# Kernel tuning notes

Hardware: AMD Instinct MI355X
Metric: run time of the kernel (lower is better)

The kernel has to match this reference:

```python
import jax, jax.numpy as jnp
import numpy as np

B, D, E, H, T = 16384, 32, 8, 64, 10  # batch, state_dim, n_experts, hidden, time points
TEMP = 1.0  # gating temperature


def setup_inputs() -> dict:
    key = jax.random.key(0)
    ks = jax.random.split(key, 12)
    w = lambda k, shape, fan_in: (jax.random.normal(k, shape, jnp.float32) / np.sqrt(fan_in)).astype(jnp.float32)
    return {
        "x0": jax.random.normal(ks[0], (B, D), jnp.float32),
        "t_span": jnp.linspace(0.0, 1.0, T).astype(jnp.float32),
        # per-expert time-conditioned MLP: (x, t) -> H -> H -> D
        "W1": w(ks[1], (E, D + 1, H), D + 1), "b1": jnp.zeros((E, H), jnp.float32),
        "W2": w(ks[2], (E, H, H), H),          "b2": jnp.zeros((E, H), jnp.float32),
        "W3": w(ks[3], (E, H, D), H),          "b3": jnp.zeros((E, D), jnp.float32),
        # gating MLP on concat(x, dx_init): 2D -> H -> E
        "Gw1": w(ks[4], (2 * D, H), 2 * D), "Gb1": jnp.zeros((H,), jnp.float32),
        "Gw2": w(ks[5], (H, E), H),         "Gb2": jnp.zeros((E,), jnp.float32),
    }


def _dyn(t, x, W1, b1, W2, b2, W3, b3, Gw1, Gb1, Gw2, Gb2):
    # AME-ODE training-path dynamics: uniform-weighted init, gate, weighted sum
    inp = jnp.concatenate([x, jnp.ones((x.shape[0], 1), x.dtype) * t], axis=-1)  # [B, D+1]
    h = jnp.tanh(jnp.einsum('bi,eih->beh', inp, W1) + b1)
    h = jnp.tanh(jnp.einsum('beh,ehg->beg', h, W2) + b2)
    f = jnp.einsum('beg,egd->bed', h, W3) + b3          # all-expert dynamics [B, E, D]
    dx_init = f.mean(axis=1)                             # uniform weights 1/E
    g = jnp.tanh(jnp.concatenate([x, dx_init], -1) @ Gw1 + Gb1)
    wgt = jax.nn.softmax((g @ Gw2 + Gb2) / TEMP, axis=-1)  # [B, E]
    return jnp.einsum('be,bed->bd', wgt, f)


def reference(x0, t_span, W1, b1, W2, b2, W3, b3, Gw1, Gb1, Gw2, Gb2):
    params = (W1, b1, W2, b2, W3, b3, Gw1, Gb1, Gw2, Gb2)

    def step(x, ts):
        t0, t1 = ts[0], ts[1]
        dt = t1 - t0
        k1 = _dyn(t0, x, *params)
        k2 = _dyn(t0 + 0.5 * dt, x + 0.5 * dt * k1, *params)
        k3 = _dyn(t0 + 0.5 * dt, x + 0.5 * dt * k2, *params)
        k4 = _dyn(t1, x + dt * k3, *params)
        xn = x + (dt / 6.0) * (k1 + 2.0 * k2 + 2.0 * k3 + k4)
        return xn, xn

    pairs = jnp.stack([t_span[:-1], t_span[1:]], axis=1)  # [T-1, 2]
    _, traj = jax.lax.scan(step, x0, pairs)               # [T-1, B, D]
    traj = jnp.concatenate([x0[None], traj], axis=0)       # [T, B, D]
    return jnp.transpose(traj, (1, 0, 2))                  # [B, T, D]
```

## Files before the change

kernel.cpp:

```cpp
#include <hip/hip_runtime.h>
#include <hip/hip_bf16.h>

typedef unsigned int u32;
typedef unsigned short u16;
typedef __attribute__((ext_vector_type(8))) short short8;
typedef __attribute__((ext_vector_type(4))) float f32x4;
typedef __attribute__((ext_vector_type(4))) u32 u32x4;
typedef __attribute__((ext_vector_type(2))) u32 u32x2;

#define DD 32
#define EE 8
#define HH 64
#define TT 10
#define BATCH 16384
#define EPB 64
#define DYN_LDS 75776

#if __has_builtin(__builtin_amdgcn_exp2f)
#define EXP2F(x) __builtin_amdgcn_exp2f(x)
#else
#define EXP2F(x) __builtin_exp2f(x)
#endif

__device__ __forceinline__ float fast_tanh(float x) {
  float e = EXP2F(x * 2.885390082f);
  return 1.f - 2.f * __builtin_amdgcn_rcpf(e + 1.f);
}
__device__ __forceinline__ u16 f2b_rn(float v) {
  return (u16)((__float_as_uint(v) + 0x8000u) >> 16);
}
__device__ __forceinline__ u32 pack2_rn(float a, float b) {
  return __builtin_amdgcn_perm(__float_as_uint(b) + 0x8000u,
                               __float_as_uint(a) + 0x8000u, 0x07060302u);
}
__device__ __forceinline__ float unp_lo(u32 p) { return __uint_as_float(p << 16); }
__device__ __forceinline__ float unp_hi(u32 p) { return __uint_as_float(p & 0xffff0000u); }
__device__ __forceinline__ short8 lds_frag(const u32* p) {
  u32x4 v = *(const u32x4*)p;
  return __builtin_bit_cast(short8, v);
}
__device__ __forceinline__ f32x4 bcast4(float v) { f32x4 c; c[0]=v; c[1]=v; c[2]=v; c[3]=v; return c; }

__global__ __launch_bounds__(512) void ame_ode_kernel(
    const float* __restrict__ x0, const float* __restrict__ tspan,
    const float* __restrict__ W1, const float* __restrict__ b1,
    const float* __restrict__ W2, const float* __restrict__ b2,
    const float* __restrict__ W3, const float* __restrict__ b3,
    const float* __restrict__ Gw1, const float* __restrict__ Gb1,
    const float* __restrict__ Gw2, const float* __restrict__ Gb2,
    float* __restrict__ out)
{
  extern __shared__ __align__(16) u32 dynbuf[];
  u32*  const xdb = dynbuf;
  u32*  const fsb = dynbuf + 1280;
  u32*  const hs  = dynbuf + 9728;

  const int tid  = threadIdx.x;
  const int lane = tid & 63;
  const int l15  = lane & 15;
  const int quad = lane >> 4;
  const int e    = __builtin_amdgcn_readfirstlane(tid >> 6);

  const int el = lane >> 3;
  const int q8 = lane & 7;
  const int gr = e * 8 + el;
  const int gb = blockIdx.x * EPB + gr;

  const float* W1f = W1 + e * (DD + 1) * HH;
  const float* b1f = b1 + e * HH;
  const float* W2f = W2 + e * HH * HH;
  const float* b2f = b2 + e * HH;
  const float* W3f = W3 + e * HH * DD;
  const float* b3f = b3 + e * DD;

  short8 bw1[4], bw2[2][4], bw3[2][2];
  #pragma unroll
  for (int nt = 0; nt < 4; nt++)
    #pragma unroll
    for (int j = 0; j < 8; j++)
      bw1[nt][j] = (short)f2b_rn(W1f[(quad * 8 + j) * HH + nt * 16 + l15]);
  #pragma unroll
  for (int ks = 0; ks < 2; ks++)
    #pragma unroll
    for (int nt = 0; nt < 4; nt++)
      #pragma unroll
      for (int j = 0; j < 8; j++)
        bw2[ks][nt][j] = (short)f2b_rn(W2f[(ks * 32 + quad * 8 + j) * HH + nt * 16 + l15]);
  #pragma unroll
  for (int ks = 0; ks < 2; ks++)
    #pragma unroll
    for (int dt2 = 0; dt2 < 2; dt2++)
      #pragma unroll
      for (int j = 0; j < 8; j++)
        bw3[ks][dt2][j] = (short)f2b_rn(W3f[(ks * 32 + quad * 8 + j) * DD + dt2 * 16 + l15]);

  short8 bg1x[4], bg1f[4];
  float gb1v[4];
  #pragma unroll
  for (int nt = 0; nt < 4; nt++) {
    #pragma unroll
    for (int j = 0; j < 8; j++) {
      bg1x[nt][j] = (short)f2b_rn(Gw1[(quad * 8 + j) * HH + nt * 16 + l15]);
      bg1f[nt][j] = (short)f2b_rn(0.125f * Gw1[(DD + quad * 8 + j) * HH + nt * 16 + l15]);
    }
    gb1v[nt] = Gb1[nt * 16 + l15];
  }

  short8 bg2[2];
  #pragma unroll
  for (int ks = 0; ks < 2; ks++)
    #pragma unroll
    for (int j = 0; j < 8; j++)
      bg2[ks][j] = (short)((l15 < 8) ? f2b_rn(Gw2[(ks * 32 + quad * 8 + j) * EE + l15]) : 0);
  const float gb2v = (l15 < 8) ? Gb2[l15] : 0.f;

  u32 c1p[4], c2p[2], c3p;
  #pragma unroll
  for (int nt = 0; nt < 4; nt++)
    c1p[nt] = pack2_rn(b1f[nt * 16 + l15], W1f[DD * HH + nt * 16 + l15]);
  #pragma unroll
  for (int p = 0; p < 2; p++)
    c2p[p] = pack2_rn(b2f[(2 * p) * 16 + l15], b2f[(2 * p + 1) * 16 + l15]);
  c3p = pack2_rn(b3f[l15], b3f[16 + l15]);

  float xst[4], xacc[4];
  {
    const float4 v = *(const float4*)(x0 + gb * DD + q8 * 4);
    xst[0] = v.x; xst[1] = v.y; xst[2] = v.z; xst[3] = v.w;
    xacc[0] = v.x; xacc[1] = v.y; xacc[2] = v.z; xacc[3] = v.w;
    u32x2 p; p.x = pack2_rn(v.x, v.y); p.y = pack2_rn(v.z, v.w);
    *(u32x2*)&xdb[gr * 20 + q8 * 2] = p;
    *(float4*)(out + gb * TT * DD + q8 * 4) = v;
  }
  __syncthreads();

  u16*  const fw16 = (u16*)fsb;
  u32*  const hsw  = hs + e * 1152;
  u16*  const uw16 = (u16*)hsw;
  float* const wscr = (float*)(hsw + 576);

  #pragma unroll 1
  for (int step = 0; step < TT - 1; step++) {
    const float t0 = tspan[step];
    const float t1 = tspan[step + 1];
    const float dt = t1 - t0;

    #pragma unroll 1
    for (int s = 0; s < 4; s++) {
      const float tcur = (s == 0) ? t0 : ((s == 3) ? t1 : t0 + 0.5f * dt);

      f32x4 c1i[4];
      #pragma unroll
      for (int nt = 0; nt < 4; nt++)
        c1i[nt] = bcast4(__builtin_fmaf(tcur, unp_hi(c1p[nt]), unp_lo(c1p[nt])));

      #pragma unroll 2
      for (int mt = 0; mt < 4; mt++) {
        u32* const hw   = hsw + (mt & 1) * 576;
        u16* const hw16 = (u16*)hw;

        const short8 a1 = lds_frag(&xdb[(mt * 16 + l15) * 20 + quad * 4]);
        f32x4 h1a[4];
        #pragma unroll
        for (int nt = 0; nt < 4; nt++)
          h1a[nt] = __builtin_amdgcn_mfma_f32_16x16x32_bf16(a1, bw1[nt], c1i[nt], 0, 0, 0);
        #pragma unroll
        for (int nt = 0; nt < 4; nt++)
          #pragma unroll
          for (int r = 0; r < 4; r++)
            hw16[(quad * 4 + r) * 72 + nt * 16 + l15] = f2b_rn(fast_tanh(h1a[nt][r]));

        f32x4 h2a[4];
        #pragma unroll
        for (int nt = 0; nt < 4; nt++)
          h2a[nt] = bcast4((nt & 1) ? unp_hi(c2p[nt >> 1]) : unp_lo(c2p[nt >> 1]));
        #pragma unroll
        for (int ks = 0; ks < 2; ks++) {
          const short8 a2 = lds_frag(&hw[l15 * 36 + ks * 16 + quad * 4]);
          #pragma unroll
          for (int nt = 0; nt < 4; nt++)
            h2a[nt] = __builtin_amdgcn_mfma_f32_16x16x32_bf16(a2, bw2[ks][nt], h2a[nt], 0, 0, 0);
        }
        #pragma unroll
        for (int nt = 0; nt < 4; nt++)
          #pragma unroll
          for (int r = 0; r < 4; r++)
            hw16[(quad * 4 + r) * 72 + nt * 16 + l15] = f2b_rn(fast_tanh(h2a[nt][r]));

        f32x4 fa[2];
        #pragma unroll
        for (int dt2 = 0; dt2 < 2; dt2++)
          fa[dt2] = bcast4(dt2 ? unp_hi(c3p) : unp_lo(c3p));
        #pragma unroll
        for (int ks = 0; ks < 2; ks++) {
          const short8 a3 = lds_frag(&hw[l15 * 36 + ks * 16 + quad * 4]);
          #pragma unroll
          for (int dt2 = 0; dt2 < 2; dt2++)
            fa[dt2] = __builtin_amdgcn_mfma_f32_16x16x32_bf16(a3, bw3[ks][dt2], fa[dt2], 0, 0, 0);
        }
        #pragma unroll
        for (int dt2 = 0; dt2 < 2; dt2++)
          #pragma unroll
          for (int r = 0; r < 4; r++)
            fw16[(mt * 16 + quad * 4 + r) * 264 + e * 32 + dt2 * 16 + l15] = f2b_rn(fa[dt2][r]);
      }

      f32x4 u4[4];
      {
        const short8 ax = lds_frag(&xdb[(e * 8 + (l15 & 7)) * 20 + quad * 4]);
        #pragma unroll
        for (int nt = 0; nt < 4; nt++)
          u4[nt] = __builtin_amdgcn_mfma_f32_16x16x32_bf16(ax, bg1x[nt], bcast4(gb1v[nt]), 0, 0, 0);
      }
      __syncthreads();

      #pragma unroll
      for (int kb = 0; kb < 8; kb++) {
        const short8 af = lds_frag(&fsb[(e * 8 + (l15 & 7)) * 132 + kb * 16 + quad * 4]);
        #pragma unroll
        for (int nt = 0; nt < 4; nt++)
          u4[nt] = __builtin_amdgcn_mfma_f32_16x16x32_bf16(af, bg1f[nt], u4[nt], 0, 0, 0);
      }
      #pragma unroll
      for (int nt = 0; nt < 4; nt++)
        #pragma unroll
        for (int r = 0; r < 4; r++)
          uw16[(quad * 4 + r) * 72 + nt * 16 + l15] = f2b_rn(fast_tanh(u4[nt][r]));

      f32x4 lv = bcast4(gb2v);
      #pragma unroll
      for (int ks = 0; ks < 2; ks++) {
        const short8 ag = lds_frag(&hsw[l15 * 36 + ks * 16 + quad * 4]);
        lv = __builtin_amdgcn_mfma_f32_16x16x32_bf16(ag, bg2[ks], lv, 0, 0, 0);
      }

      float wgt[4];
      #pragma unroll
      for (int r = 0; r < 4; r++) {
        const float p = __expf(lv[r]);
        float ssum = p + __shfl_xor(p, 1);
        ssum += __shfl_xor(ssum, 2);
        ssum += __shfl_xor(ssum, 4);
        wgt[r] = p * __builtin_amdgcn_rcpf(ssum);
      }
      if (quad < 2 && l15 < 8) {
        #pragma unroll
        for (int r = 0; r < 4; r++)
          wscr[(quad * 4 + r) * 8 + l15] = wgt[r];
      }
      const f32x4 w0 = *(const f32x4*)&wscr[el * 8];
      const f32x4 w1 = *(const f32x4*)&wscr[el * 8 + 4];

      float kc[4] = {0.f, 0.f, 0.f, 0.f};
      #pragma unroll
      for (int j = 0; j < EE; j++) {
        const float wg = (j < 4) ? w0[j] : w1[j - 4];
        const u32x2 pf = *(const u32x2*)&fsb[gr * 132 + j * 16 + q8 * 2];
        kc[0] = __builtin_fmaf(wg, unp_lo(pf.x), kc[0]);
        kc[1] = __builtin_fmaf(wg, unp_hi(pf.x), kc[1]);
        kc[2] = __builtin_fmaf(wg, unp_lo(pf.y), kc[2]);
        kc[3] = __builtin_fmaf(wg, unp_hi(pf.y), kc[3]);
      }

      const float wk = (s == 1 || s == 2) ? 2.f : 1.f;
      const float ak = dt * (1.f / 6.f) * wk;
      #pragma unroll
      for (int q = 0; q < 4; q++) xacc[q] = __builtin_fmaf(ak, kc[q], xacc[q]);

      float xn[4];
      if (s < 3) {
        const float cn = (s == 2) ? dt : 0.5f * dt;
        #pragma unroll
        for (int q = 0; q < 4; q++) xn[q] = __builtin_fmaf(cn, kc[q], xst[q]);
      } else {
        #pragma unroll
        for (int q = 0; q < 4; q++) { xst[q] = xacc[q]; xn[q] = xacc[q]; }
        float4 o; o.x = xn[0]; o.y = xn[1]; o.z = xn[2]; o.w = xn[3];
        *(float4*)(out + (gb * TT + step + 1) * DD + q8 * 4) = o;
      }
      u32x2 p; p.x = pack2_rn(xn[0], xn[1]); p.y = pack2_rn(xn[2], xn[3]);
      *(u32x2*)&xdb[gr * 20 + q8 * 2] = p;

      __syncthreads();
    }
  }
}

extern "C" void kernel_launch(void* const* d_in, const int* in_sizes, int n_in,
                              void* d_out, int out_size, void* d_ws, size_t ws_size,
                              hipStream_t stream)
{
  const float* x0    = (const float*)d_in[0];
  const float* tspan = (const float*)d_in[1];
  const float* W1  = (const float*)d_in[2];
  const float* b1  = (const float*)d_in[3];
  const float* W2  = (const float*)d_in[4];
  const float* b2  = (const float*)d_in[5];
  const float* W3  = (const float*)d_in[6];
  const float* b3  = (const float*)d_in[7];
  const float* Gw1 = (const float*)d_in[8];
  const float* Gb1 = (const float*)d_in[9];
  const float* Gw2 = (const float*)d_in[10];
  const float* Gb2 = (const float*)d_in[11];

  (void)hipFuncSetAttribute((const void*)ame_ode_kernel,
                            hipFuncAttributeMaxDynamicSharedMemorySize, DYN_LDS);

  ame_ode_kernel<<<BATCH / EPB, 512, DYN_LDS, stream>>>(
      x0, tspan, W1, b1, W2, b2, W3, b3, Gw1, Gb1, Gw2, Gb2, (float*)d_out);
}
```

Measured before the change: 343.5 us.

## Repartition gating GEMM across warps to remove redundant row computation

Before, each warp computed the gating first layer for 16 A-rows of which only 8 were real (rows l15&7 duplicated), across all 4 N-tiles. Now each of the 8 warps computes one 16-row M-tile by two N-tiles of the gating hidden layer. The results go to a new shared LDS buffer, and after an extra barrier each warp reads its rows back for the second gating layer. This halves the redundant MFMA work and the gating weight registers, at the cost of an added __syncthreads and more LDS.

```diff
diff --git a/kernel.cpp b/kernel.cpp
--- a/kernel.cpp
+++ b/kernel.cpp
@@ -14,7 +14,7 @@
 #define TT 10
 #define BATCH 16384
 #define EPB 64
-#define DYN_LDS 75776
+#define DYN_LDS 84992
 
 #if __has_builtin(__builtin_amdgcn_exp2f)
 #define EXP2F(x) __builtin_amdgcn_exp2f(x)
@@ -53,7 +53,8 @@
   extern __shared__ __align__(16) u32 dynbuf[];
   u32*  const xdb = dynbuf;
   u32*  const fsb = dynbuf + 1280;
-  u32*  const hs  = dynbuf + 9728;
+  u32*  const usb = dynbuf + 9728;
+  u32*  const hs  = dynbuf + 12032;
 
   const int tid  = threadIdx.x;
   const int lane = tid & 63;
@@ -94,17 +95,18 @@
       for (int j = 0; j < 8; j++)
         bw3[ks][dt2][j] = (short)f2b_rn(W3f[(ks * 32 + quad * 8 + j) * DD + dt2 * 16 + l15]);
 
-  short8 bg1x[4], bg1f[4];
-  float gb1v[4];
-  #pragma unroll
-  for (int nt = 0; nt < 4; nt++) {
+  const int g1mt = e & 3;
+  const int g1n0 = (e >> 2) * 2;
+  short8 bg1x[2], bg1f[2];
+  #pragma unroll
+  for (int ni = 0; ni < 2; ni++)
     #pragma unroll
     for (int j = 0; j < 8; j++) {
-      bg1x[nt][j] = (short)f2b_rn(Gw1[(quad * 8 + j) * HH + nt * 16 + l15]);
-      bg1f[nt][j] = (short)f2b_rn(0.125f * Gw1[(DD + quad * 8 + j) * HH + nt * 16 + l15]);
+      bg1x[ni][j] = (short)f2b_rn(Gw1[(quad * 8 + j) * HH + (g1n0 + ni) * 16 + l15]);
+      bg1f[ni][j] = (short)f2b_rn(0.125f * Gw1[(DD + quad * 8 + j) * HH + (g1n0 + ni) * 16 + l15]);
     }
-    gb1v[nt] = Gb1[nt * 16 + l15];
-  }
+  const float gb1a = Gb1[g1n0 * 16 + l15];
+  const float gb1b = Gb1[(g1n0 + 1) * 16 + l15];
 
   short8 bg2[2];
   #pragma unroll
@@ -125,19 +127,18 @@
 
   float xst[4], xacc[4];
   {
-    const float4 v = *(const float4*)(x0 + gb * DD + q8 * 4);
+    const float4 v = *(const float4*)(x0 + gb * DD + 4 * q8);
     xst[0] = v.x; xst[1] = v.y; xst[2] = v.z; xst[3] = v.w;
     xacc[0] = v.x; xacc[1] = v.y; xacc[2] = v.z; xacc[3] = v.w;
     u32x2 p; p.x = pack2_rn(v.x, v.y); p.y = pack2_rn(v.z, v.w);
     *(u32x2*)&xdb[gr * 20 + q8 * 2] = p;
-    *(float4*)(out + gb * TT * DD + q8 * 4) = v;
+    *(float4*)(out + gb * TT * DD + 4 * q8) = v;
   }
   __syncthreads();
 
-  u16*  const fw16 = (u16*)fsb;
-  u32*  const hsw  = hs + e * 1152;
-  u16*  const uw16 = (u16*)hsw;
-  float* const wscr = (float*)(hsw + 576);
+  u16* const fw16 = (u16*)fsb;
+  u16* const us16 = (u16*)usb;
+  u32* const hsw  = hs + e * 1152;
 
   #pragma unroll 1
   for (int step = 0; step < TT - 1; step++) {
@@ -204,83 +205,83 @@
           for (int r = 0; r < 4; r++)
             fw16[(mt * 16 + quad * 4 + r) * 264 + e * 32 + dt2 * 16 + l15] = f2b_rn(fa[dt2][r]);
       }
-
-      f32x4 u4[4];
+      __syncthreads();
+
       {
-        const short8 ax = lds_frag(&xdb[(e * 8 + (l15 & 7)) * 20 + quad * 4]);
-        #pragma unroll
-        for (int nt = 0; nt < 4; nt++)
-          u4[nt] = __builtin_amdgcn_mfma_f32_16x16x32_bf16(ax, bg1x[nt], bcast4(gb1v[nt]), 0, 0, 0);
+        f32x4 u0 = bcast4(gb1a), u1 = bcast4(gb1b);
+        const int mg = g1mt * 16 + l15;
+        const short8 ax = lds_frag(&xdb[mg * 20 + quad * 4]);
+        u0 = __builtin_amdgcn_mfma_f32_16x16x32_bf16(ax, bg1x[0], u0, 0, 0, 0);
+        u1 = __builtin_amdgcn_mfma_f32_16x16x32_bf16(ax, bg1x[1], u1, 0, 0, 0);
+        #pragma unroll
+        for (int kb = 0; kb < 8; kb++) {
+          const short8 af = lds_frag(&fsb[mg * 132 + kb * 16 + quad * 4]);
+          u0 = __builtin_amdgcn_mfma_f32_16x16x32_bf16(af, bg1f[0], u0, 0, 0, 0);
+          u1 = __builtin_amdgcn_mfma_f32_16x16x32_bf16(af, bg1f[1], u1, 0, 0, 0);
+        }
+        #pragma unroll
+        for (int r = 0; r < 4; r++) {
+          us16[(g1mt * 16 + quad * 4 + r) * 72 + g1n0 * 16 + l15]       = f2b_rn(fast_tanh(u0[r]));
+          us16[(g1mt * 16 + quad * 4 + r) * 72 + (g1n0 + 1) * 16 + l15] = f2b_rn(fast_tanh(u1[r]));
+        }
       }
       __syncthreads();
 
-      #pragma unroll
-      for (int kb = 0; kb < 8; kb++) {
-        const short8 af = lds_frag(&fsb[(e * 8 + (l15 & 7)) * 132 + kb * 16 + quad * 4]);
-        #pragma unroll
-        for (int nt = 0; nt < 4; nt++)
-          u4[nt] = __builtin_amdgcn_mfma_f32_16x16x32_bf16(af, bg1f[nt], u4[nt], 0, 0, 0);
+      {
+        f32x4 lv = bcast4(gb2v);
+        #pragma unroll
+        for (int ks = 0; ks < 2; ks++) {
+          const short8 ag = lds_frag(&usb[(e * 8 + (l15 & 7)) * 36 + ks * 16 + quad * 4]);
+          lv = __builtin_amdgcn_mfma_f32_16x16x32_bf16(ag, bg2[ks], lv, 0, 0, 0);
+        }
+        float wgt[4];
+        #pragma unroll
+        for (int r = 0; r < 4; r++) {
+          const float p = __expf(lv[r]);
+          float ssum = p + __shfl_xor(p, 1);
+          ssum += __shfl_xor(ssum, 2);
+          ssum += __shfl_xor(ssum, 4);
+          wgt[r] = p * __builtin_amdgcn_rcpf(ssum);
+        }
+        float* const wscr = (float*)(hsw + 576);
+        if (quad < 2 && l15 < 8) {
+          #pragma unroll
+          for (int r = 0; r < 4; r++)
+            wscr[((quad * 4 + r) & 7) * 8 + l15] = wgt[r];
+        }
+        const f32x4 w0 = *(const f32x4*)&wscr[el * 8];
+        const f32x4 w1 = *(const f32x4*)&wscr[el * 8 + 4];
+
+        float kc[4] = {0.f, 0.f, 0.f, 0.f};
+        #pragma unroll
+        for (int j = 0; j < EE; j++) {
+          const float wg = (j < 4) ? w0[j] : w1[j - 4];
+          const u32x2 pf = *(const u32x2*)&fsb[gr * 132 + j * 16 + q8 * 2];
+          kc[0] = __builtin_fmaf(wg, unp_lo(pf.x), kc[0]);
+          kc[1] = __builtin_fmaf(wg, unp_hi(pf.x), kc[1]);
+          kc[2] = __builtin_fmaf(wg, unp_lo(pf.y), kc[2]);
+          kc[3] = __builtin_fmaf(wg, unp_hi(pf.y), kc[3]);
+        }
+
+        const float wk = (s == 1 || s == 2) ? 2.f : 1.f;
+        const float ak = dt * (1.f / 6.f) * wk;
+        #pragma unroll
+        for (int q = 0; q < 4; q++) xacc[q] = __builtin_fmaf(ak, kc[q], xacc[q]);
+
+        float xn[4];
+        if (s < 3) {
+          const float cn = (s == 2) ? dt : 0.5f * dt;
+          #pragma unroll
+          for (int q = 0; q < 4; q++) xn[q] = __builtin_fmaf(cn, kc[q], xst[q]);
+        } else {
+          #pragma unroll
+          for (int q = 0; q < 4; q++) { xst[q] = xacc[q]; xn[q] = xacc[q]; }
+          float4 o; o.x = xn[0]; o.y = xn[1]; o.z = xn[2]; o.w = xn[3];
+          *(float4*)(out + (gb * TT + step + 1) * DD + 4 * q8) = o;
+        }
+        u32x2 p; p.x = pack2_rn(xn[0], xn[1]); p.y = pack2_rn(xn[2], xn[3]);
+        *(u32x2*)&xdb[gr * 20 + q8 * 2] = p;
       }
-      #pragma unroll
-      for (int nt = 0; nt < 4; nt++)
-        #pragma unroll
-        for (int r = 0; r < 4; r++)
-          uw16[(quad * 4 + r) * 72 + nt * 16 + l15] = f2b_rn(fast_tanh(u4[nt][r]));
-
-      f32x4 lv = bcast4(gb2v);
-      #pragma unroll
-      for (int ks = 0; ks < 2; ks++) {
-        const short8 ag = lds_frag(&hsw[l15 * 36 + ks * 16 + quad * 4]);
-        lv = __builtin_amdgcn_mfma_f32_16x16x32_bf16(ag, bg2[ks], lv, 0, 0, 0);
-      }
-
-      float wgt[4];
-      #pragma unroll
-      for (int r = 0; r < 4; r++) {
-        const float p = __expf(lv[r]);
-        float ssum = p + __shfl_xor(p, 1);
-        ssum += __shfl_xor(ssum, 2);
-        ssum += __shfl_xor(ssum, 4);
-        wgt[r] = p * __builtin_amdgcn_rcpf(ssum);
-      }
-      if (quad < 2 && l15 < 8) {
-        #pragma unroll
-        for (int r = 0; r < 4; r++)
-          wscr[(quad * 4 + r) * 8 + l15] = wgt[r];
-      }
-      const f32x4 w0 = *(const f32x4*)&wscr[el * 8];
-      const f32x4 w1 = *(const f32x4*)&wscr[el * 8 + 4];
-
-      float kc[4] = {0.f, 0.f, 0.f, 0.f};
-      #pragma unroll
-      for (int j = 0; j < EE; j++) {
-        const float wg = (j < 4) ? w0[j] : w1[j - 4];
-        const u32x2 pf = *(const u32x2*)&fsb[gr * 132 + j * 16 + q8 * 2];
-        kc[0] = __builtin_fmaf(wg, unp_lo(pf.x), kc[0]);
-        kc[1] = __builtin_fmaf(wg, unp_hi(pf.x), kc[1]);
-        kc[2] = __builtin_fmaf(wg, unp_lo(pf.y), kc[2]);
-        kc[3] = __builtin_fmaf(wg, unp_hi(pf.y), kc[3]);
-      }
-
-      const float wk = (s == 1 || s == 2) ? 2.f : 1.f;
-      const float ak = dt * (1.f / 6.f) * wk;
-      #pragma unroll
-      for (int q = 0; q < 4; q++) xacc[q] = __builtin_fmaf(ak, kc[q], xacc[q]);
-
-      float xn[4];
-      if (s < 3) {
-        const float cn = (s == 2) ? dt : 0.5f * dt;
-        #pragma unroll
-        for (int q = 0; q < 4; q++) xn[q] = __builtin_fmaf(cn, kc[q], xst[q]);
-      } else {
-        #pragma unroll
-        for (int q = 0; q < 4; q++) { xst[q] = xacc[q]; xn[q] = xacc[q]; }
-        float4 o; o.x = xn[0]; o.y = xn[1]; o.z = xn[2]; o.w = xn[3];
-        *(float4*)(out + (gb * TT + step + 1) * DD + q8 * 4) = o;
-      }
-      u32x2 p; p.x = pack2_rn(xn[0], xn[1]); p.y = pack2_rn(xn[2], xn[3]);
-      *(u32x2*)&xdb[gr * 20 + q8 * 2] = p;
-
       __syncthreads();
     }
   }
```

Result: faster. 332.0 us (-3.3%).
